# Kernel optimization log

Hardware: AMD Instinct MI355X
Metric: run time of the kernel (lower is better)

The kernel has to match this reference:

```python
import jax, jax.numpy as jnp
import numpy as np

SPARSITY = 0.1     # fraction of elements kept per sample
MASK_BASE = 0.0    # 0.0 -> hard binary mask path


def setup_inputs() -> dict:
    key = jax.random.key(0)
    h = jax.random.normal(key, (64, 512, 32, 32), dtype=jnp.float32)
    tau = jnp.full((1,), 0.8, dtype=jnp.float32)  # blend coefficient
    return {"h": h, "tau": tau}


def reference(h, tau):
    # h: (N, C, H, W); per-sample top-k cutoff on |h| then mask-blend.
    N, C, H, W = h.shape
    chw = C * H * W
    k0 = int(SPARSITY * chw)  # 0-based index into descending sort
    a = jnp.abs(h.reshape(N, -1))
    srt = jnp.sort(a, axis=1)            # ascending sort, (N, CHW)
    cutoff = srt[:, chw - 1 - k0]        # == descending-sorted[:, k0], (N,)
    mask = (jnp.abs(h) >= cutoff[:, None, None, None]).astype(h.dtype)
    t = tau[0]
    # mask*h*tau + h*(1-tau); reduces to mask*h when tau == 1.0
    return mask * h * t + h * (1.0 - t)
```

## Files before the change

### kernel.cpp

```cpp
#include <hip/hip_runtime.h>
#include <cstdint>
#include <cstddef>

#define CHW 524288
#define F4_PER_SAMPLE (CHW / 4)
#define BLOCKS_PER_SAMPLE 64
#define F4_PER_BLOCK (F4_PER_SAMPLE / BLOCKS_PER_SAMPLE)
#define NTHREADS 256
#define F4_PER_THREAD (F4_PER_BLOCK / NTHREADS)
#define ELEMS_PER_THREAD (F4_PER_THREAD * 4)
#define NB12 4096
#define NB10 1024
#define NB7  128
#define LCAP 512
#define NTH2 1024
#define DCAP 16384
#define NBA  640
#define WIN_LO_KEY 0x3FCE0000u
#define WIN_HI_KEY 0x3FD80000u

typedef float f32x4 __attribute__((ext_vector_type(4)));

__device__ __forceinline__ unsigned int akey(float x) {
    return __float_as_uint(x) & 0x7FFFFFFFu;
}

__global__ __launch_bounds__(NTHREADS) void zero_ws(unsigned int* __restrict__ p, int words) {
    int i = blockIdx.x * NTHREADS + threadIdx.x;
    if (i < words) p[i] = 0u;
}

__device__ __forceinline__ unsigned int wave_iscan(unsigned int v, int lane) {
#pragma unroll
    for (int off = 1; off < 64; off <<= 1) {
        unsigned int u = __shfl_up(v, off);
        if (lane >= off) v += u;
    }
    return v;
}

template<int NT>
__device__ __forceinline__ void find_bin2(const unsigned int* lh, int nbins,
                                          unsigned int r,
                                          unsigned int* sbin, unsigned int* srem) {
    __shared__ unsigned int wsum[NT / 64];
    const int t = threadIdx.x, ln = t & 63, wv = t >> 6;
    const int bpt = (nbins + NT - 1) / NT;
    unsigned int s = 0;
    const int b0 = t * bpt;
#pragma unroll 4
    for (int i = 0; i < bpt; ++i) { int b = b0 + i; if (b < nbins) s += lh[b]; }
    unsigned int inc = wave_iscan(s, ln);
    if (ln == 63) wsum[wv] = inc;
    __syncthreads();
    if (wv == 0 && ln < NT / 64) {
        unsigned int x = wsum[ln];
#pragma unroll
        for (int off = 1; off < NT / 64; off <<= 1) {
            unsigned int u = __shfl_up(x, off, NT / 64);
            if (ln >= off) x += u;
        }
        wsum[ln] = x;
    }
    __syncthreads();
    const unsigned int base = (wv > 0) ? wsum[wv - 1] : 0u;
    const unsigned int excl = base + inc - s;
    if (s > 0 && r >= excl && r < excl + s) {
        unsigned int acc = excl;
        for (int i = 0; i < bpt; ++i) {
            int b = b0 + i;
            unsigned int c = (b < nbins) ? lh[b] : 0u;
            if (r < acc + c) { *sbin = (unsigned int)b; *srem = r - acc; break; }
            acc += c;
        }
    }
    __syncthreads();
}

__global__ __launch_bounds__(NTHREADS) void win_compact(const float4* __restrict__ h,
                                                        unsigned int* __restrict__ cand,
                                                        unsigned int* __restrict__ bcnt,
                                                        unsigned int* __restrict__ bchi) {
    __shared__ unsigned int lbuf[LCAP];
    __shared__ unsigned int wtot[4], wchi[4];
    const int t = threadIdx.x;
    const int lane = t & 63;
    const int w = t >> 6;
    const int bid = blockIdx.x;
    const float4* p = h + (size_t)bid * F4_PER_BLOCK;

    float4 vv[F4_PER_THREAD];
#pragma unroll
    for (int k = 0; k < F4_PER_THREAD; ++k) vv[k] = p[k * NTHREADS + t];
    unsigned int keys[ELEMS_PER_THREAD];
#pragma unroll
    for (int k = 0; k < F4_PER_THREAD; ++k) {
        keys[4 * k + 0] = akey(vv[k].x);
        keys[4 * k + 1] = akey(vv[k].y);
        keys[4 * k + 2] = akey(vv[k].z);
        keys[4 * k + 3] = akey(vv[k].w);
    }

    unsigned int chi = 0, cwin = 0;
#pragma unroll
    for (int j = 0; j < ELEMS_PER_THREAD; ++j) {
        chi  += (keys[j] >= WIN_HI_KEY) ? 1u : 0u;
        cwin += (keys[j] >= WIN_LO_KEY && keys[j] < WIN_HI_KEY) ? 1u : 0u;
    }

    unsigned int inc = wave_iscan(cwin, lane);
    unsigned int wc = chi;
#pragma unroll
    for (int off = 32; off > 0; off >>= 1) wc += __shfl_xor(wc, off);

    if (lane == 63) wtot[w] = inc;
    if (lane == 0)  wchi[w] = wc;
    __syncthreads();

    unsigned int wbase = 0;
#pragma unroll
    for (int i = 0; i < 4; ++i) if (i < w) wbase += wtot[i];
    const unsigned int total  = wtot[0] + wtot[1] + wtot[2] + wtot[3];
    const unsigned int chitot = wchi[0] + wchi[1] + wchi[2] + wchi[3];
    unsigned int pos = wbase + inc - cwin;

#pragma unroll
    for (int j = 0; j < ELEMS_PER_THREAD; ++j) {
        unsigned int key = keys[j];
        if (key >= WIN_LO_KEY && key < WIN_HI_KEY) {
            if (pos < (unsigned int)LCAP) lbuf[pos] = key;
            ++pos;
        }
    }
    __syncthreads();

    if (t == 0) { bcnt[bid] = total; bchi[bid] = chitot; }
    const unsigned int wcnt = (total < (unsigned int)LCAP) ? total : (unsigned int)LCAP;
    unsigned int* mycand = cand + (size_t)bid * LCAP;
    for (unsigned int i = t; i < wcnt; i += NTHREADS) mycand[i] = lbuf[i];
}

__global__ __launch_bounds__(NTH2) void select_cand(const unsigned int* __restrict__ cand,
                                                    const unsigned int* __restrict__ bcnt,
                                                    const unsigned int* __restrict__ bchi,
                                                    const float* __restrict__ h,
                                                    unsigned int* __restrict__ cutk,
                                                    unsigned int need_total,
                                                    unsigned int rank) {
    __shared__ unsigned int dense[DCAP];
    __shared__ unsigned int lh[NB10];
    __shared__ unsigned int cnts[64], excl[64];
    __shared__ unsigned int sb1, sr1, sb2, sr2, sb3, sr3;
    __shared__ unsigned int s_ovf, s_cn, s_chi;
    const int n = blockIdx.x;
    const int t = threadIdx.x;

    if (t < 64) {
        unsigned int c  = bcnt[(n << 6) + t];
        unsigned int ch = bchi[(n << 6) + t];
        cnts[t] = c;
        unsigned long long m = __ballot(c > (unsigned int)LCAP);
        unsigned int inc = wave_iscan(c, t);
        excl[t] = inc - c;
        unsigned int chs = ch;
#pragma unroll
        for (int off = 32; off > 0; off >>= 1) chs += __shfl_xor(chs, off);
        if (t == 63) s_cn = inc;
        if (t == 0) { s_chi = chs; s_ovf = (m != 0ull) ? 1u : 0u; }
    }
    __syncthreads();
    const unsigned int cn  = s_cn;
    const unsigned int chi = s_chi;
    const bool in_win = (s_ovf == 0u) && (cn <= (unsigned int)DCAP) &&
                        (chi < need_total) && (chi + cn >= need_total);

    if (in_win) {
        const int wv = t >> 6, ln = t & 63;
        for (int j = 0; j < 4; ++j) {
            const int c = wv + (j << 4);
            const unsigned int bc  = cnts[c];
            const unsigned int off = excl[c];
            const unsigned int* src = cand + (size_t)((n << 6) + c) * LCAP;
            for (unsigned int i = ln; i < bc; i += 64) dense[off + i] = src[i];
        }
        for (int i = t; i < NBA; i += NTH2) lh[i] = 0;
        __syncthreads();
        const unsigned int rp = cn - (need_total - chi);

        for (unsigned int i = t; i < cn; i += NTH2)
            atomicAdd(&lh[(dense[i] - WIN_LO_KEY) >> 10], 1u);
        __syncthreads();
        find_bin2<NTH2>(lh, NBA, rp, &sb1, &sr1);
        const unsigned int cb = sb1, r2 = sr1;

        for (int i = t; i < NB10; i += NTH2) lh[i] = 0;
        __syncthreads();
        for (unsigned int i = t; i < cn; i += NTH2) {
            unsigned int wv2 = dense[i] - WIN_LO_KEY;
            if ((wv2 >> 10) == cb) atomicAdd(&lh[wv2 & 0x3FFu], 1u);
        }
        __syncthreads();
        find_bin2<NTH2>(lh, NB10, r2, &sb2, &sr2);
        if (t == 0) cutk[n] = WIN_LO_KEY + (cb << 10) + sb2;
        return;
    }

    const float* hp = h + (size_t)n * CHW;
    unsigned int* lhF = dense;

    for (int i = t; i < NB12; i += NTH2) lhF[i] = 0;
    __syncthreads();
    for (unsigned int i = t; i < (unsigned int)CHW; i += NTH2)
        atomicAdd(&lhF[akey(hp[i]) >> 19], 1u);
    __syncthreads();
    find_bin2<NTH2>(lhF, NB12, rank, &sb1, &sr1);
    const unsigned int b1 = sb1, r1 = sr1;

    for (int i = t; i < NB12; i += NTH2) lhF[i] = 0;
    __syncthreads();
    for (unsigned int i = t; i < (unsigned int)CHW; i += NTH2) {
        unsigned int key = akey(hp[i]);
        if ((key >> 19) == b1) atomicAdd(&lhF[(key >> 7) & 0xFFFu], 1u);
    }
    __syncthreads();
    find_bin2<NTH2>(lhF, NB12, r1, &sb2, &sr2);
    const unsigned int b2 = sb2, r2f = sr2;
    const unsigned int p24 = (b1 << 12) | b2;

    for (int i = t; i < NB7; i += NTH2) lhF[i] = 0;
    __syncthreads();
    for (unsigned int i = t; i < (unsigned int)CHW; i += NTH2) {
        unsigned int key = akey(hp[i]);
        if ((key >> 7) == p24) atomicAdd(&lhF[key & 0x7Fu], 1u);
    }
    __syncthreads();
    find_bin2<NTH2>(lhF, NB7, r2f, &sb3, &sr3);
    if (t == 0) cutk[n] = (p24 << 7) | sb3;
}

__global__ __launch_bounds__(NTHREADS) void apply_kernel(const f32x4* __restrict__ h,
                                                         const float* __restrict__ tau,
                                                         const unsigned int* __restrict__ cutoff,
                                                         f32x4* __restrict__ out) {
    const int n = blockIdx.x >> 6;
    const int chunk = blockIdx.x & 63;
    const unsigned int c = cutoff[n];
    const float t = tau[0];
    const float lo = 1.0f - t;
    const size_t base = (size_t)n * F4_PER_SAMPLE + (size_t)chunk * F4_PER_BLOCK;
    const int tid = threadIdx.x;
#pragma unroll
    for (int k = 0; k < F4_PER_THREAD; ++k) {
        f32x4 v = h[base + k * NTHREADS + tid];
        f32x4 o;
        o.x = v.x * ((akey(v.x) >= c) ? 1.0f : lo);
        o.y = v.y * ((akey(v.y) >= c) ? 1.0f : lo);
        o.z = v.z * ((akey(v.z) >= c) ? 1.0f : lo);
        o.w = v.w * ((akey(v.w) >= c) ? 1.0f : lo);
        out[base + k * NTHREADS + tid] = o;
    }
}

__global__ __launch_bounds__(NTHREADS) void hist_pass1(const float4* __restrict__ h,
                                                       unsigned int* __restrict__ hist) {
    __shared__ unsigned int lh[NB12];
    const int t = threadIdx.x;
    for (int i = t; i < NB12; i += NTHREADS) lh[i] = 0;
    __syncthreads();
    const float4* p = h + (size_t)blockIdx.x * F4_PER_BLOCK;
    const int n = blockIdx.x >> 6;
#pragma unroll
    for (int k = 0; k < F4_PER_THREAD; ++k) {
        float4 v = p[k * NTHREADS + t];
        atomicAdd(&lh[akey(v.x) >> 19], 1u);
        atomicAdd(&lh[akey(v.y) >> 19], 1u);
        atomicAdd(&lh[akey(v.z) >> 19], 1u);
        atomicAdd(&lh[akey(v.w) >> 19], 1u);
    }
    __syncthreads();
    unsigned int* gh = hist + (size_t)n * NB12;
    for (int i = t; i < NB12; i += NTHREADS) {
        unsigned int v = lh[i];
        if (v) atomicAdd(&gh[i], v);
    }
}

__global__ __launch_bounds__(NTHREADS) void hist_pass2(const float4* __restrict__ h,
                                                       const unsigned int* __restrict__ state_bits,
                                                       unsigned int* __restrict__ hist) {
    __shared__ unsigned int lh[NB12];
    const int t = threadIdx.x;
    for (int i = t; i < NB12; i += NTHREADS) lh[i] = 0;
    __syncthreads();
    const int n = blockIdx.x >> 6;
    const unsigned int b1 = state_bits[n];
    const float4* p = h + (size_t)blockIdx.x * F4_PER_BLOCK;
#pragma unroll
    for (int k = 0; k < F4_PER_THREAD; ++k) {
        float4 v = p[k * NTHREADS + t];
        unsigned int ka = akey(v.x), kb = akey(v.y), kc = akey(v.z), kd = akey(v.w);
        if ((ka >> 19) == b1) atomicAdd(&lh[(ka >> 7) & 0xFFFu], 1u);
        if ((kb >> 19) == b1) atomicAdd(&lh[(kb >> 7) & 0xFFFu], 1u);
        if ((kc >> 19) == b1) atomicAdd(&lh[(kc >> 7) & 0xFFFu], 1u);
        if ((kd >> 19) == b1) atomicAdd(&lh[(kd >> 7) & 0xFFFu], 1u);
    }
    __syncthreads();
    unsigned int* gh = hist + (size_t)n * NB12;
    for (int i = t; i < NB12; i += NTHREADS) {
        unsigned int v = lh[i];
        if (v) atomicAdd(&gh[i], v);
    }
}

__global__ __launch_bounds__(NTHREADS) void hist_pass3(const float4* __restrict__ h,
                                                       const unsigned int* __restrict__ state_bits,
                                                       unsigned int* __restrict__ hist) {
    __shared__ unsigned int lh[NB7];
    const int t = threadIdx.x;
    for (int i = t; i < NB7; i += NTHREADS) lh[i] = 0;
    __syncthreads();
    const int n = blockIdx.x >> 6;
    const unsigned int p24 = state_bits[n];
    const float4* p = h + (size_t)blockIdx.x * F4_PER_BLOCK;
#pragma unroll
    for (int k = 0; k < F4_PER_THREAD; ++k) {
        float4 v = p[k * NTHREADS + t];
        unsigned int ka = akey(v.x), kb = akey(v.y), kc = akey(v.z), kd = akey(v.w);
        if ((ka >> 7) == p24) atomicAdd(&lh[ka & 0x7Fu], 1u);
        if ((kb >> 7) == p24) atomicAdd(&lh[kb & 0x7Fu], 1u);
        if ((kc >> 7) == p24) atomicAdd(&lh[kc & 0x7Fu], 1u);
        if ((kd >> 7) == p24) atomicAdd(&lh[kd & 0x7Fu], 1u);
    }
    __syncthreads();
    unsigned int* gh = hist + (size_t)n * NB7;
    for (int i = t; i < NB7; i += NTHREADS) {
        unsigned int v = lh[i];
        if (v) atomicAdd(&gh[i], v);
    }
}

__global__ __launch_bounds__(NTH2) void select_pass(const unsigned int* __restrict__ hist,
                                                    int nbins, int pass,
                                                    unsigned int* __restrict__ state_bits,
                                                    unsigned int* __restrict__ state_rank,
                                                    unsigned int* __restrict__ cutoff,
                                                    unsigned int init_rank) {
    __shared__ unsigned int sbin, srem;
    const int n = blockIdx.x;
    const int t = threadIdx.x;
    const unsigned int* gh = hist + (size_t)n * nbins;
    const unsigned int r = (pass == 0) ? init_rank : state_rank[n];
    find_bin2<NTH2>(gh, nbins, r, &sbin, &srem);
    if (t == 0) {
        if (pass == 0) { state_bits[n] = sbin; state_rank[n] = srem; }
        else if (pass == 1) { state_bits[n] = (state_bits[n] << 12) | sbin; state_rank[n] = srem; }
        else { cutoff[n] = (state_bits[n] << 7) | sbin; }
    }
}

extern "C" void kernel_launch(void* const* d_in, const int* in_sizes, int n_in,
                              void* d_out, int out_size, void* d_ws, size_t ws_size,
                              hipStream_t stream) {
    const float* h = (const float*)d_in[0];
    const float* tau = (const float*)d_in[1];
    float* out = (float*)d_out;

    const int total = in_sizes[0];
    const int N = total / CHW;
    const int NBLK = N * BLOCKS_PER_SAMPLE;

    const int k0 = (int)(0.1 * (double)CHW);
    const unsigned int init_rank = (unsigned int)(CHW - 1 - k0);
    const unsigned int need_total = (unsigned int)CHW - init_rank;

    dim3 grid((unsigned)NBLK), blk(NTHREADS);

    const size_t fast_words = 2 * (size_t)NBLK + (size_t)N + (size_t)NBLK * LCAP;
    if (ws_size >= fast_words * 4) {
        unsigned int* bcnt = (unsigned int*)d_ws;
        unsigned int* bchi = bcnt + NBLK;
        unsigned int* cutk = bchi + NBLK;
        unsigned int* cand = cutk + N;

        win_compact<<<grid, blk, 0, stream>>>((const float4*)h, cand, bcnt, bchi);
        select_cand<<<N, NTH2, 0, stream>>>(cand, bcnt, bchi, h, cutk,
                                            need_total, init_rank);
        apply_kernel<<<grid, blk, 0, stream>>>((const f32x4*)h, tau, cutk, (f32x4*)out);
        return;
    }

    unsigned int* hist1 = (unsigned int*)d_ws;
    unsigned int* hist2 = hist1 + (size_t)N * NB12;
    unsigned int* hist3 = hist2 + (size_t)N * NB12;
    unsigned int* sbits = hist3 + (size_t)N * NB7;
    unsigned int* srank = sbits + N;
    unsigned int* cutk  = srank + N;
    const int zwords = 2 * N * NB12 + N * NB7 + 3 * N;

    zero_ws<<<(zwords + NTHREADS - 1) / NTHREADS, blk, 0, stream>>>(hist1, zwords);
    hist_pass1<<<grid, blk, 0, stream>>>((const float4*)h, hist1);
    select_pass<<<N, NTH2, 0, stream>>>(hist1, NB12, 0, sbits, srank, cutk, init_rank);
    hist_pass2<<<grid, blk, 0, stream>>>((const float4*)h, sbits, hist2);
    select_pass<<<N, NTH2, 0, stream>>>(hist2, NB12, 1, sbits, srank, cutk, 0u);
    hist_pass3<<<grid, blk, 0, stream>>>((const float4*)h, sbits, hist3);
    select_pass<<<N, NTH2, 0, stream>>>(hist3, NB7, 2, sbits, srank, cutk, 0u);
    apply_kernel<<<grid, blk, 0, stream>>>((const f32x4*)h, tau, cutk, (f32x4*)out);
}
```

Before: 76.22 us.

## Fuse speculative apply into compaction pass and patch window candidates afterward

The compaction kernel now also writes the output speculatively: values above the window's high key keep their full value and all others get the (1-tau) factor. It stores each window candidate's raw bits and position, and a fixup kernel afterwards rewrites only the candidates at or above the final cutoff. This removes the second full read of h and full write of out that the separate apply kernel did, leaving a sparse scatter in the common case. The cost is an extra position buffer and smaller per-block candidate capacity (LCAP 512 to 256), which makes the slow full-apply fallback more likely. The speculative path also returns v[c] unscaled for masked-in elements, which matches the reference only when mask*h*tau + h*(1-tau) equals h, so this is exact up to rounding.

Result: faster. 67.18 us (-11.9%).

```diff
diff --git a/kernel.cpp b/kernel.cpp
--- a/kernel.cpp
+++ b/kernel.cpp
@@ -8,11 +8,10 @@
 #define F4_PER_BLOCK (F4_PER_SAMPLE / BLOCKS_PER_SAMPLE)
 #define NTHREADS 256
 #define F4_PER_THREAD (F4_PER_BLOCK / NTHREADS)
-#define ELEMS_PER_THREAD (F4_PER_THREAD * 4)
 #define NB12 4096
 #define NB10 1024
 #define NB7  128
-#define LCAP 512
+#define LCAP 256
 #define NTH2 1024
 #define DCAP 16384
 #define NBA  640
@@ -77,46 +76,50 @@
     __syncthreads();
 }
 
-__global__ __launch_bounds__(NTHREADS) void win_compact(const float4* __restrict__ h,
-                                                        unsigned int* __restrict__ cand,
-                                                        unsigned int* __restrict__ bcnt,
-                                                        unsigned int* __restrict__ bchi) {
-    __shared__ unsigned int lbuf[LCAP];
+__global__ __launch_bounds__(NTHREADS) void fused_compact_apply(
+        const f32x4* __restrict__ h, const float* __restrict__ tau,
+        f32x4* __restrict__ out,
+        unsigned int* __restrict__ cvb, unsigned int* __restrict__ cpo,
+        unsigned int* __restrict__ bcnt, unsigned int* __restrict__ bchi) {
+    __shared__ unsigned int lvb[LCAP], lpo[LCAP];
     __shared__ unsigned int wtot[4], wchi[4];
-    const int t = threadIdx.x;
-    const int lane = t & 63;
-    const int w = t >> 6;
-    const int bid = blockIdx.x;
-    const float4* p = h + (size_t)bid * F4_PER_BLOCK;
-
-    float4 vv[F4_PER_THREAD];
+    const int t = threadIdx.x, lane = t & 63, w = t >> 6, bid = blockIdx.x;
+    const f32x4* p = h + (size_t)bid * F4_PER_BLOCK;
+    f32x4* q = out + (size_t)bid * F4_PER_BLOCK;
+    const float tv = tau[0];
+    const float lo = 1.0f - tv;
+
+    f32x4 vv[F4_PER_THREAD];
 #pragma unroll
     for (int k = 0; k < F4_PER_THREAD; ++k) vv[k] = p[k * NTHREADS + t];
-    unsigned int keys[ELEMS_PER_THREAD];
-#pragma unroll
-    for (int k = 0; k < F4_PER_THREAD; ++k) {
-        keys[4 * k + 0] = akey(vv[k].x);
-        keys[4 * k + 1] = akey(vv[k].y);
-        keys[4 * k + 2] = akey(vv[k].z);
-        keys[4 * k + 3] = akey(vv[k].w);
-    }
 
     unsigned int chi = 0, cwin = 0;
 #pragma unroll
-    for (int j = 0; j < ELEMS_PER_THREAD; ++j) {
-        chi  += (keys[j] >= WIN_HI_KEY) ? 1u : 0u;
-        cwin += (keys[j] >= WIN_LO_KEY && keys[j] < WIN_HI_KEY) ? 1u : 0u;
+    for (int k = 0; k < F4_PER_THREAD; ++k) {
+#pragma unroll
+        for (int c = 0; c < 4; ++c) {
+            unsigned int key = akey(vv[k][c]);
+            chi  += (key >= WIN_HI_KEY) ? 1u : 0u;
+            cwin += (key >= WIN_LO_KEY && key < WIN_HI_KEY) ? 1u : 0u;
+        }
+    }
+
+#pragma unroll
+    for (int k = 0; k < F4_PER_THREAD; ++k) {
+        f32x4 v = vv[k], o;
+#pragma unroll
+        for (int c = 0; c < 4; ++c)
+            o[c] = (akey(v[c]) >= WIN_HI_KEY) ? v[c] : v[c] * lo;
+        q[k * NTHREADS + t] = o;
     }
 
     unsigned int inc = wave_iscan(cwin, lane);
     unsigned int wc = chi;
 #pragma unroll
     for (int off = 32; off > 0; off >>= 1) wc += __shfl_xor(wc, off);
-
     if (lane == 63) wtot[w] = inc;
     if (lane == 0)  wchi[w] = wc;
     __syncthreads();
-
     unsigned int wbase = 0;
 #pragma unroll
     for (int i = 0; i < 4; ++i) if (i < w) wbase += wtot[i];
@@ -125,26 +128,35 @@
     unsigned int pos = wbase + inc - cwin;
 
 #pragma unroll
-    for (int j = 0; j < ELEMS_PER_THREAD; ++j) {
-        unsigned int key = keys[j];
-        if (key >= WIN_LO_KEY && key < WIN_HI_KEY) {
-            if (pos < (unsigned int)LCAP) lbuf[pos] = key;
-            ++pos;
+    for (int k = 0; k < F4_PER_THREAD; ++k) {
+#pragma unroll
+        for (int c = 0; c < 4; ++c) {
+            unsigned int b = __float_as_uint(vv[k][c]);
+            unsigned int key = b & 0x7FFFFFFFu;
+            if (key >= WIN_LO_KEY && key < WIN_HI_KEY) {
+                if (pos < (unsigned int)LCAP) {
+                    lvb[pos] = b;
+                    lpo[pos] = (unsigned int)(((k * NTHREADS + t) << 2) | c);
+                }
+                ++pos;
+            }
         }
     }
     __syncthreads();
 
     if (t == 0) { bcnt[bid] = total; bchi[bid] = chitot; }
     const unsigned int wcnt = (total < (unsigned int)LCAP) ? total : (unsigned int)LCAP;
-    unsigned int* mycand = cand + (size_t)bid * LCAP;
-    for (unsigned int i = t; i < wcnt; i += NTHREADS) mycand[i] = lbuf[i];
-}
-
-__global__ __launch_bounds__(NTH2) void select_cand(const unsigned int* __restrict__ cand,
+    unsigned int* mvb = cvb + (size_t)bid * LCAP;
+    unsigned int* mpo = cpo + (size_t)bid * LCAP;
+    for (unsigned int i = t; i < wcnt; i += NTHREADS) { mvb[i] = lvb[i]; mpo[i] = lpo[i]; }
+}
+
+__global__ __launch_bounds__(NTH2) void select_cand(const unsigned int* __restrict__ cvb,
                                                     const unsigned int* __restrict__ bcnt,
                                                     const unsigned int* __restrict__ bchi,
                                                     const float* __restrict__ h,
                                                     unsigned int* __restrict__ cutk,
+                                                    unsigned int* __restrict__ flags,
                                                     unsigned int need_total,
                                                     unsigned int rank) {
     __shared__ unsigned int dense[DCAP];
@@ -180,8 +192,8 @@
             const int c = wv + (j << 4);
             const unsigned int bc  = cnts[c];
             const unsigned int off = excl[c];
-            const unsigned int* src = cand + (size_t)((n << 6) + c) * LCAP;
-            for (unsigned int i = ln; i < bc; i += 64) dense[off + i] = src[i];
+            const unsigned int* src = cvb + (size_t)((n << 6) + c) * LCAP;
+            for (unsigned int i = ln; i < bc; i += 64) dense[off + i] = src[i] & 0x7FFFFFFFu;
         }
         for (int i = t; i < NBA; i += NTH2) lh[i] = 0;
         __syncthreads();
@@ -201,7 +213,7 @@
         }
         __syncthreads();
         find_bin2<NTH2>(lh, NB10, r2, &sb2, &sr2);
-        if (t == 0) cutk[n] = WIN_LO_KEY + (cb << 10) + sb2;
+        if (t == 0) { cutk[n] = WIN_LO_KEY + (cb << 10) + sb2; flags[n] = 1u; }
         return;
     }
 
@@ -235,29 +247,43 @@
     }
     __syncthreads();
     find_bin2<NTH2>(lhF, NB7, r2f, &sb3, &sr3);
-    if (t == 0) cutk[n] = (p24 << 7) | sb3;
-}
-
-__global__ __launch_bounds__(NTHREADS) void apply_kernel(const f32x4* __restrict__ h,
-                                                         const float* __restrict__ tau,
-                                                         const unsigned int* __restrict__ cutoff,
-                                                         f32x4* __restrict__ out) {
-    const int n = blockIdx.x >> 6;
-    const int chunk = blockIdx.x & 63;
-    const unsigned int c = cutoff[n];
-    const float t = tau[0];
-    const float lo = 1.0f - t;
-    const size_t base = (size_t)n * F4_PER_SAMPLE + (size_t)chunk * F4_PER_BLOCK;
-    const int tid = threadIdx.x;
-#pragma unroll
-    for (int k = 0; k < F4_PER_THREAD; ++k) {
-        f32x4 v = h[base + k * NTHREADS + tid];
-        f32x4 o;
-        o.x = v.x * ((akey(v.x) >= c) ? 1.0f : lo);
-        o.y = v.y * ((akey(v.y) >= c) ? 1.0f : lo);
-        o.z = v.z * ((akey(v.z) >= c) ? 1.0f : lo);
-        o.w = v.w * ((akey(v.w) >= c) ? 1.0f : lo);
-        out[base + k * NTHREADS + tid] = o;
+    if (t == 0) { cutk[n] = (p24 << 7) | sb3; flags[n] = 0u; }
+}
+
+__global__ __launch_bounds__(NTHREADS) void fixup(const f32x4* __restrict__ h,
+                                                  const float* __restrict__ tau,
+                                                  const unsigned int* __restrict__ cvb,
+                                                  const unsigned int* __restrict__ cpo,
+                                                  const unsigned int* __restrict__ bcnt,
+                                                  const unsigned int* __restrict__ cutk,
+                                                  const unsigned int* __restrict__ flags,
+                                                  float* __restrict__ outf,
+                                                  f32x4* __restrict__ outv) {
+    const int bid = blockIdx.x, t = threadIdx.x, n = bid >> 6;
+    const unsigned int cut = cutk[n];
+    if (flags[n] != 0u) {
+        unsigned int cnt = bcnt[bid];
+        if (cnt > (unsigned int)LCAP) cnt = (unsigned int)LCAP;
+        const unsigned int* vb = cvb + (size_t)bid * LCAP;
+        const unsigned int* po = cpo + (size_t)bid * LCAP;
+        const size_t ebase = (size_t)bid * (F4_PER_BLOCK * 4);
+        for (unsigned int i = t; i < cnt; i += NTHREADS) {
+            unsigned int b = vb[i];
+            if ((b & 0x7FFFFFFFu) >= cut) outf[ebase + po[i]] = __uint_as_float(b);
+        }
+    } else {
+        const float tv = tau[0];
+        const float lo = 1.0f - tv;
+        const f32x4* p = h + (size_t)bid * F4_PER_BLOCK;
+        f32x4* q = outv + (size_t)bid * F4_PER_BLOCK;
+#pragma unroll
+        for (int k = 0; k < F4_PER_THREAD; ++k) {
+            f32x4 v = p[k * NTHREADS + t], o;
+#pragma unroll
+            for (int c = 0; c < 4; ++c)
+                o[c] = (akey(v[c]) >= cut) ? v[c] : v[c] * lo;
+            q[k * NTHREADS + t] = o;
+        }
     }
 }
 
@@ -358,6 +384,29 @@
     }
 }
 
+__global__ __launch_bounds__(NTHREADS) void apply_kernel(const f32x4* __restrict__ h,
+                                                         const float* __restrict__ tau,
+                                                         const unsigned int* __restrict__ cutoff,
+                                                         f32x4* __restrict__ out) {
+    const int n = blockIdx.x >> 6;
+    const int chunk = blockIdx.x & 63;
+    const unsigned int c = cutoff[n];
+    const float t = tau[0];
+    const float lo = 1.0f - t;
+    const size_t base = (size_t)n * F4_PER_SAMPLE + (size_t)chunk * F4_PER_BLOCK;
+    const int tid = threadIdx.x;
+#pragma unroll
+    for (int k = 0; k < F4_PER_THREAD; ++k) {
+        f32x4 v = h[base + k * NTHREADS + tid];
+        f32x4 o;
+        o.x = v.x * ((akey(v.x) >= c) ? 1.0f : lo);
+        o.y = v.y * ((akey(v.y) >= c) ? 1.0f : lo);
+        o.z = v.z * ((akey(v.z) >= c) ? 1.0f : lo);
+        o.w = v.w * ((akey(v.w) >= c) ? 1.0f : lo);
+        out[base + k * NTHREADS + tid] = o;
+    }
+}
+
 extern "C" void kernel_launch(void* const* d_in, const int* in_sizes, int n_in,
                               void* d_out, int out_size, void* d_ws, size_t ws_size,
                               hipStream_t stream) {
@@ -375,17 +424,21 @@
 
     dim3 grid((unsigned)NBLK), blk(NTHREADS);
 
-    const size_t fast_words = 2 * (size_t)NBLK + (size_t)N + (size_t)NBLK * LCAP;
+    const size_t fast_words = 2 * (size_t)NBLK + 2 * (size_t)N + 2 * (size_t)NBLK * LCAP;
     if (ws_size >= fast_words * 4) {
-        unsigned int* bcnt = (unsigned int*)d_ws;
-        unsigned int* bchi = bcnt + NBLK;
-        unsigned int* cutk = bchi + NBLK;
-        unsigned int* cand = cutk + N;
-
-        win_compact<<<grid, blk, 0, stream>>>((const float4*)h, cand, bcnt, bchi);
-        select_cand<<<N, NTH2, 0, stream>>>(cand, bcnt, bchi, h, cutk,
+        unsigned int* bcnt  = (unsigned int*)d_ws;
+        unsigned int* bchi  = bcnt + NBLK;
+        unsigned int* cutk  = bchi + NBLK;
+        unsigned int* flags = cutk + N;
+        unsigned int* cvb   = flags + N;
+        unsigned int* cpo   = cvb + (size_t)NBLK * LCAP;
+
+        fused_compact_apply<<<grid, blk, 0, stream>>>((const f32x4*)h, tau, (f32x4*)out,
+                                                      cvb, cpo, bcnt, bchi);
+        select_cand<<<N, NTH2, 0, stream>>>(cvb, bcnt, bchi, h, cutk, flags,
                                             need_total, init_rank);
-        apply_kernel<<<grid, blk, 0, stream>>>((const f32x4*)h, tau, cutk, (f32x4*)out);
+        fixup<<<grid, blk, 0, stream>>>((const f32x4*)h, tau, cvb, cpo, bcnt,
+                                        cutk, flags, out, (f32x4*)out);
         return;
     }
 
```
